# Optimization experiments

Hardware: AMD Instinct MI355X
Metric: run time of the kernel (lower is better)

The kernel has to match this reference:

```python
import jax, jax.numpy as jnp
import numpy as np

NUM_HOPS = 3
SIGMA = 0.1
EPS = 1e-12  # torch F.normalize default eps


def _l2_normalize(v):
    n = jnp.linalg.norm(v, axis=1, keepdims=True)
    return v / jnp.maximum(n, EPS)


def setup_inputs() -> dict:
    key = jax.random.key(0)
    k1, k2 = jax.random.split(key)
    N, d, E = 50000, 128, 500000
    x = jax.random.normal(k1, (N, d), dtype=jnp.float32)
    edge_index = jax.random.randint(k2, (2, E), 0, N, dtype=jnp.int64)
    return {"x": x, "edge_index": edge_index}


def reference(x, edge_index):
    N = x.shape[0]
    src, dst = edge_index[0], edge_index[1]
    noise_key = jax.random.key(42)
    h = _l2_normalize(x)
    outs = [h]
    for k in range(NUM_HOPS):
        h_src = h[src]                              # [E, d] gather
        h_dst = h[dst]                              # [E, d] gather
        alpha = jax.nn.sigmoid(jnp.sum(h_src * h_dst, axis=1))  # [E]
        # sparse.mm(alpha^T, h): out[dst] += alpha_e * h[src]
        aggr = jax.ops.segment_sum(alpha[:, None] * h_src, dst, num_segments=N)
        noise = SIGMA * jax.random.normal(jax.random.fold_in(noise_key, k), aggr.shape, aggr.dtype)
        h = _l2_normalize(aggr + noise)
        outs.append(h)
    return jnp.stack(outs)  # [num_hops+1, N, d]
```

## Files before the change

### kernel.cpp

```cpp
#include <hip/hip_runtime.h>
#include <stdint.h>

#define D 128
#define SIGMA 0.1f

typedef unsigned int uint;
typedef unsigned short ushort;

__host__ __device__ inline void tf2x32(uint32_t k0, uint32_t k1,
                                       uint32_t x0, uint32_t x1,
                                       uint32_t& o0, uint32_t& o1) {
  const uint32_t ks2 = k0 ^ k1 ^ 0x1BD11BDAu;
#define ROTL(v, r) (((v) << (r)) | ((v) >> (32 - (r))))
#define RND(R) { x0 += x1; x1 = ROTL(x1, R); x1 ^= x0; }
  x0 += k0; x1 += k1;
  RND(13) RND(15) RND(26) RND(6)
  x0 += k1; x1 += ks2 + 1u;
  RND(17) RND(29) RND(16) RND(24)
  x0 += ks2; x1 += k0 + 2u;
  RND(13) RND(15) RND(26) RND(6)
  x0 += k0; x1 += k1 + 3u;
  RND(17) RND(29) RND(16) RND(24)
  x0 += k1; x1 += ks2 + 4u;
  RND(13) RND(15) RND(26) RND(6)
  x0 += ks2; x1 += k0 + 5u;
#undef RND
#undef ROTL
  o0 = x0; o1 = x1;
}

__device__ inline float jax_normal(uint32_t k0, uint32_t k1, uint32_t idx) {
  uint32_t o0, o1;
  tf2x32(k0, k1, 0u, idx, o0, o1);
  uint32_t bits = o0 ^ o1;
  float f = __uint_as_float((bits >> 9) | 0x3f800000u) - 1.0f;
  const float lo = __uint_as_float(0xBF7FFFFFu);
  float u = fmaxf(lo, f * 2.0f + lo);
  float w = -__logf((1.0f - u) * (1.0f + u));
  float p;
  if (w < 5.0f) {
    w -= 2.5f;
    p = 2.81022636e-08f;
    p = fmaf(p, w, 3.43273939e-07f);
    p = fmaf(p, w, -3.5233877e-06f);
    p = fmaf(p, w, -4.39150654e-06f);
    p = fmaf(p, w, 0.00021858087f);
    p = fmaf(p, w, -0.00125372503f);
    p = fmaf(p, w, -0.00417768164f);
    p = fmaf(p, w, 0.246640727f);
    p = fmaf(p, w, 1.50140941f);
  } else {
    w = sqrtf(w) - 3.0f;
    p = -0.000200214257f;
    p = fmaf(p, w, 0.000100950558f);
    p = fmaf(p, w, 0.00134934322f);
    p = fmaf(p, w, -0.00367342844f);
    p = fmaf(p, w, 0.00573950773f);
    p = fmaf(p, w, -0.0076224613f);
    p = fmaf(p, w, 0.00943887047f);
    p = fmaf(p, w, 1.00167406f);
    p = fmaf(p, w, 2.83297682f);
  }
  return 1.41421356237f * (p * u);
}

__device__ inline uint bf16r(float f) {
  uint u = __float_as_uint(f);
  return (u + 0x7fffu + ((u >> 16) & 1u)) >> 16;
}

__device__ inline void unpk8(uint4 u, float* a) {
  a[0] = __uint_as_float(u.x << 16);
  a[1] = __uint_as_float(u.x & 0xffff0000u);
  a[2] = __uint_as_float(u.y << 16);
  a[3] = __uint_as_float(u.y & 0xffff0000u);
  a[4] = __uint_as_float(u.z << 16);
  a[5] = __uint_as_float(u.z & 0xffff0000u);
  a[6] = __uint_as_float(u.w << 16);
  a[7] = __uint_as_float(u.w & 0xffff0000u);
}

template<int USEB>
__device__ inline void ldrow16(const float* __restrict__ hf,
                               const uint4* __restrict__ hb,
                               int node, int sl, float* a) {
  if (USEB) {
    unpk8(hb[node * 16 + sl], a);
  } else {
    float4 v0 = ((const float4*)hf)[node * 32 + sl * 2];
    float4 v1 = ((const float4*)hf)[node * 32 + sl * 2 + 1];
    a[0] = v0.x; a[1] = v0.y; a[2] = v0.z; a[3] = v0.w;
    a[4] = v1.x; a[5] = v1.y; a[6] = v1.z; a[7] = v1.w;
  }
}

__global__ __launch_bounds__(256) void k_hist(const int* __restrict__ dst,
                                              int* __restrict__ cnt, int E) {
  int i = (blockIdx.x * blockDim.x + threadIdx.x) * 4;
  if (i + 3 < E) {
    int4 d = *(const int4*)(dst + i);
    atomicAdd(&cnt[d.x], 1);
    atomicAdd(&cnt[d.y], 1);
    atomicAdd(&cnt[d.z], 1);
    atomicAdd(&cnt[d.w], 1);
  } else {
    for (int j = i; j < E; ++j) atomicAdd(&cnt[dst[j]], 1);
  }
}

__global__ __launch_bounds__(256) void k_bsum(const int* __restrict__ cnt,
                                              int* __restrict__ bsum, int N) {
  __shared__ int ws[4];
  int b = blockIdx.x, t = threadIdx.x;
  int base = b * 1024 + t * 4;
  int4 c = {0, 0, 0, 0};
  if (base + 3 < N) c = *(const int4*)(cnt + base);
  else {
    if (base < N) c.x = cnt[base];
    if (base + 1 < N) c.y = cnt[base + 1];
    if (base + 2 < N) c.z = cnt[base + 2];
    if (base + 3 < N) c.w = cnt[base + 3];
  }
  int s = c.x + c.y + c.z + c.w;
  #pragma unroll
  for (int off = 32; off; off >>= 1) s += __shfl_xor(s, off);
  if ((t & 63) == 0) ws[t >> 6] = s;
  __syncthreads();
  if (t == 0) bsum[b] = ws[0] + ws[1] + ws[2] + ws[3];
}

__global__ void k_bscan(const int* __restrict__ bsum, int* __restrict__ boff,
                        int* __restrict__ rowN, int NB) {
  int lane = threadIdx.x;
  int carry = 0;
  for (int base = 0; base < NB; base += 64) {
    int idx = base + lane;
    int v = (idx < NB) ? bsum[idx] : 0;
    int incl = v;
    #pragma unroll
    for (int off = 1; off < 64; off <<= 1) {
      int t = __shfl_up(incl, off);
      if (lane >= off) incl += t;
    }
    if (idx < NB) boff[idx] = carry + incl - v;
    carry += __shfl(incl, 63);
  }
  if (lane == 0) rowN[0] = carry;
}

__global__ __launch_bounds__(256) void k_apply(const int* __restrict__ cnt,
                                               const int* __restrict__ boff,
                                               int* __restrict__ row,
                                               int* __restrict__ cur, int N) {
  __shared__ int wsum[4];
  int b = blockIdx.x, t = threadIdx.x;
  int base = b * 1024 + t * 4;
  int4 c = {0, 0, 0, 0};
  if (base + 3 < N) c = *(const int4*)(cnt + base);
  else {
    if (base < N) c.x = cnt[base];
    if (base + 1 < N) c.y = cnt[base + 1];
    if (base + 2 < N) c.z = cnt[base + 2];
    if (base + 3 < N) c.w = cnt[base + 3];
  }
  int s = c.x + c.y + c.z + c.w;
  int incl = s;
  #pragma unroll
  for (int off = 1; off < 64; off <<= 1) {
    int tv = __shfl_up(incl, off);
    if ((t & 63) >= off) incl += tv;
  }
  int wid = t >> 6;
  if ((t & 63) == 63) wsum[wid] = incl;
  __syncthreads();
  int woff = 0;
  for (int w = 0; w < wid; ++w) woff += wsum[w];
  int ex = boff[b] + woff + incl - s;
  int r0 = ex, r1 = ex + c.x, r2 = r1 + c.y, r3 = r2 + c.z;
  if (base + 3 < N) {
    *(int4*)(row + base) = make_int4(r0, r1, r2, r3);
    *(int4*)(cur + base) = make_int4(r0, r1, r2, r3);
  } else {
    if (base < N)     { row[base] = r0;     cur[base] = r0; }
    if (base + 1 < N) { row[base + 1] = r1; cur[base + 1] = r1; }
    if (base + 2 < N) { row[base + 2] = r2; cur[base + 2] = r2; }
  }
}

__global__ __launch_bounds__(256) void k_fill(const int* __restrict__ src,
                                              const int* __restrict__ dst,
                                              int* __restrict__ cur,
                                              int* __restrict__ csr, int E) {
  int i = (blockIdx.x * blockDim.x + threadIdx.x) * 4;
  if (i + 3 < E) {
    int4 d = *(const int4*)(dst + i);
    int4 s = *(const int4*)(src + i);
    csr[atomicAdd(&cur[d.x], 1)] = s.x;
    csr[atomicAdd(&cur[d.y], 1)] = s.y;
    csr[atomicAdd(&cur[d.z], 1)] = s.z;
    csr[atomicAdd(&cur[d.w], 1)] = s.w;
  } else {
    for (int j = i; j < E; ++j) csr[atomicAdd(&cur[dst[j]], 1)] = src[j];
  }
}

template<int USEB>
__global__ __launch_bounds__(256) void k_norm0(const float* __restrict__ x,
                                               float* __restrict__ h,
                                               uint2* __restrict__ hb, int N) {
  int gid = blockIdx.x * blockDim.x + threadIdx.x;
  int node = gid >> 5, lane = gid & 31;
  if (node >= N) return;
  float4 v = ((const float4*)x)[node * 32 + lane];
  float ss = v.x * v.x + v.y * v.y + v.z * v.z + v.w * v.w;
  #pragma unroll
  for (int off = 16; off; off >>= 1) ss += __shfl_xor(ss, off);
  float inv = 1.0f / fmaxf(sqrtf(ss), 1e-12f);
  float4 o; o.x = v.x * inv; o.y = v.y * inv; o.z = v.z * inv; o.w = v.w * inv;
  ((float4*)h)[node * 32 + lane] = o;
  if (USEB) {
    uint2 u;
    u.x = bf16r(o.x) | (bf16r(o.y) << 16);
    u.y = bf16r(o.z) | (bf16r(o.w) << 16);
    hb[node * 32 + lane] = u;
  }
}

template<int USEB>
__global__ __launch_bounds__(256) void k_hop(
    const float* __restrict__ hpf, const uint4* __restrict__ hpb,
    float* __restrict__ hof, uint* __restrict__ hob, int wb,
    const int* __restrict__ row, const int* __restrict__ csr,
    int N, uint32_t k0, uint32_t k1) {
  int gid = blockIdx.x * blockDim.x + threadIdx.x;
  int node = gid >> 6;
  if (node >= N) return;
  int lane = threadIdx.x & 63;
  int sl = lane & 15, g = lane >> 4;

  float hv[8];
  ldrow16<USEB>(hpf, hpb, node, sl, hv);
  float acc[8] = {0.f, 0.f, 0.f, 0.f, 0.f, 0.f, 0.f, 0.f};

  int b = row[node], e = row[node + 1];
  for (int cb = b; cb < e; cb += 64) {
    int cn = min(64, e - cb);
    int eidx = csr[min(cb + lane, e - 1)];
    for (int jb = 0; jb < cn; jb += 16) {
      int pos = jb + (g << 2);
      int i0 = __shfl(eidx, pos);
      int i1 = __shfl(eidx, pos + 1);
      int i2 = __shfl(eidx, pos + 2);
      int i3 = __shfl(eidx, pos + 3);
      float a0[8], a1[8], a2[8], a3[8];
      ldrow16<USEB>(hpf, hpb, i0, sl, a0);
      ldrow16<USEB>(hpf, hpb, i1, sl, a1);
      ldrow16<USEB>(hpf, hpb, i2, sl, a2);
      ldrow16<USEB>(hpf, hpb, i3, sl, a3);
      float p0 = 0.f, p1 = 0.f, p2 = 0.f, p3 = 0.f;
      #pragma unroll
      for (int t = 0; t < 8; ++t) {
        p0 = fmaf(a0[t], hv[t], p0);
        p1 = fmaf(a1[t], hv[t], p1);
        p2 = fmaf(a2[t], hv[t], p2);
        p3 = fmaf(a3[t], hv[t], p3);
      }
      #pragma unroll
      for (int off = 1; off < 16; off <<= 1) {
        p0 += __shfl_xor(p0, off);
        p1 += __shfl_xor(p1, off);
        p2 += __shfl_xor(p2, off);
        p3 += __shfl_xor(p3, off);
      }
      float al0 = (pos     < cn) ? __builtin_amdgcn_rcpf(1.0f + __expf(-p0)) : 0.f;
      float al1 = (pos + 1 < cn) ? __builtin_amdgcn_rcpf(1.0f + __expf(-p1)) : 0.f;
      float al2 = (pos + 2 < cn) ? __builtin_amdgcn_rcpf(1.0f + __expf(-p2)) : 0.f;
      float al3 = (pos + 3 < cn) ? __builtin_amdgcn_rcpf(1.0f + __expf(-p3)) : 0.f;
      #pragma unroll
      for (int t = 0; t < 8; ++t) {
        acc[t] = fmaf(al0, a0[t], acc[t]);
        acc[t] = fmaf(al1, a1[t], acc[t]);
        acc[t] = fmaf(al2, a2[t], acc[t]);
        acc[t] = fmaf(al3, a3[t], acc[t]);
      }
    }
  }

  #pragma unroll
  for (int t = 0; t < 8; ++t) {
    acc[t] += __shfl_xor(acc[t], 16);
    acc[t] += __shfl_xor(acc[t], 32);
  }

  float p0s = (g & 1) ? acc[2] : acc[0];
  float p1s = (g & 1) ? acc[3] : acc[1];
  float q0s = (g & 1) ? acc[6] : acc[4];
  float q1s = (g & 1) ? acc[7] : acc[5];
  float s0 = (g & 2) ? q0s : p0s;
  float s1 = (g & 2) ? q1s : p1s;

  uint32_t j0 = (uint32_t)node * 128u + (uint32_t)sl * 8u + (uint32_t)g * 2u;
  s0 += SIGMA * jax_normal(k0, k1, j0);
  s1 += SIGMA * jax_normal(k0, k1, j0 + 1u);

  float ss = s0 * s0 + s1 * s1;
  #pragma unroll
  for (int off = 32; off; off >>= 1) ss += __shfl_xor(ss, off);
  float inv = __builtin_amdgcn_rcpf(fmaxf(sqrtf(ss), 1e-12f));
  float o0 = s0 * inv, o1 = s1 * inv;
  int oi = node * 64 + sl * 4 + g;
  ((float2*)hof)[oi] = make_float2(o0, o1);
  if (USEB && wb) hob[oi] = bf16r(o0) | (bf16r(o1) << 16);
}

extern "C" void kernel_launch(void* const* d_in, const int* in_sizes, int n_in,
                              void* d_out, int out_size, void* d_ws, size_t ws_size,
                              hipStream_t stream) {
  const float* x = (const float*)d_in[0];
  const int* ei = (const int*)d_in[1];
  int N = in_sizes[0] / D;
  int E = in_sizes[1] / 2;
  const int* src = ei;
  const int* dst = ei + E;
  float* out = (float*)d_out;
  size_t nd = (size_t)N * D;

  int Np = (N + 3) & ~3;
  int Ep = (E + 3) & ~3;
  int NB = (N + 1023) / 1024;
  int NBp = (NB + 3) & ~3;
  int* cnt  = (int*)d_ws;
  int* row  = cnt + Np;
  int* cur  = row + Np + 4;
  int* csr  = cur + Np;
  int* bsum = csr + Ep;
  int* boff = bsum + NBp;

  size_t int_bytes = ((size_t)(3 * Np + 4 + Ep + 2 * NBp)) * 4;
  size_t hb_off = (int_bytes + 255) & ~(size_t)255;
  size_t hb_bytes = (size_t)N * D * 2;
  bool useb = ws_size >= hb_off + 2 * hb_bytes;
  ushort* hb0 = (ushort*)((char*)d_ws + hb_off);
  ushort* hb1 = hb0 + (size_t)N * D;

  hipMemsetAsync(cnt, 0, sizeof(int) * (size_t)Np, stream);
  int eb4 = (E / 4 + 256) / 256;
  k_hist<<<eb4, 256, 0, stream>>>(dst, cnt, E);
  k_bsum<<<NB, 256, 0, stream>>>(cnt, bsum, N);
  k_bscan<<<1, 64, 0, stream>>>(bsum, boff, row + N, NB);
  k_apply<<<NB, 256, 0, stream>>>(cnt, boff, row, cur, N);
  k_fill<<<eb4, 256, 0, stream>>>(src, dst, cur, csr, E);

  int nb32 = (N * 32 + 255) / 256;
  int nb64 = (N * 64 + 255) / 256;

  if (useb) {
    k_norm0<1><<<nb32, 256, 0, stream>>>(x, out, (uint2*)hb0, N);
    for (int k = 0; k < 3; ++k) {
      uint32_t ka, kb;
      tf2x32(0u, 42u, 0u, (uint32_t)k, ka, kb);
      const uint4* hin = (const uint4*)((k & 1) ? hb1 : hb0);
      uint* hout = (uint*)((k & 1) ? hb0 : hb1);
      k_hop<1><<<nb64, 256, 0, stream>>>(nullptr, hin,
                                         out + (size_t)(k + 1) * nd, hout,
                                         (k < 2) ? 1 : 0,
                                         row, csr, N, ka, kb);
    }
  } else {
    k_norm0<0><<<nb32, 256, 0, stream>>>(x, out, nullptr, N);
    for (int k = 0; k < 3; ++k) {
      uint32_t ka, kb;
      tf2x32(0u, 42u, 0u, (uint32_t)k, ka, kb);
      k_hop<0><<<nb64, 256, 0, stream>>>(out + (size_t)k * nd, nullptr,
                                         out + (size_t)(k + 1) * nd, nullptr, 0,
                                         row, csr, N, ka, kb);
    }
  }
}
```

Measured before the change: 199.3 us.

## Compute edge attention dots with bf16 MFMA and fuse CSR scan kernels

The per-edge dot products in the hop kernel now run on the 16x16x32 bf16 MFMA instruction. Each chunk loads 16 neighbour rows as the A operand and the node's row as B, replacing per-lane FMAs and shuffle reductions. The neighbour rows are also loaded a second time in a per-lane layout for the weighted accumulation, which doubles gather traffic per chunk. Separately, the block scan and apply kernels are fused into one kernel when there are at most 64 blocks, and the memset is replaced by a zeroing kernel, cutting launch count in the CSR build.

```diff
diff --git a/kernel.cpp b/kernel.cpp
--- a/kernel.cpp
+++ b/kernel.cpp
@@ -6,6 +6,11 @@
 
 typedef unsigned int uint;
 typedef unsigned short ushort;
+
+typedef short s8v __attribute__((ext_vector_type(8)));
+typedef float f32x4 __attribute__((ext_vector_type(4)));
+
+union U4S8 { uint4 u; s8v s; };
 
 __host__ __device__ inline void tf2x32(uint32_t k0, uint32_t k1,
                                        uint32_t x0, uint32_t x1,
@@ -94,6 +99,11 @@
   }
 }
 
+__global__ __launch_bounds__(256) void k_zero(int4* __restrict__ p, int n4) {
+  int i = blockIdx.x * blockDim.x + threadIdx.x;
+  if (i < n4) p[i] = make_int4(0, 0, 0, 0);
+}
+
 __global__ __launch_bounds__(256) void k_hist(const int* __restrict__ dst,
                                               int* __restrict__ cnt, int E) {
   int i = (blockIdx.x * blockDim.x + threadIdx.x) * 4;
@@ -127,6 +137,60 @@
   if ((t & 63) == 0) ws[t >> 6] = s;
   __syncthreads();
   if (t == 0) bsum[b] = ws[0] + ws[1] + ws[2] + ws[3];
+}
+
+__global__ __launch_bounds__(256) void k_apply2(const int* __restrict__ cnt,
+                                                const int* __restrict__ bsum,
+                                                int* __restrict__ row,
+                                                int* __restrict__ cur,
+                                                int N, int NB) {
+  __shared__ int sboff;
+  __shared__ int wsum[4];
+  int b = blockIdx.x, t = threadIdx.x;
+  if (t < 64) {
+    int v = (t < NB) ? bsum[t] : 0;
+    int incl = v;
+    #pragma unroll
+    for (int off = 1; off < 64; off <<= 1) {
+      int tv = __shfl_up(incl, off);
+      if (t >= off) incl += tv;
+    }
+    if (t == b) sboff = incl - v;
+    if (b == 0 && t == NB - 1) row[N] = incl;
+  }
+  __syncthreads();
+
+  int base = b * 1024 + t * 4;
+  int4 c = {0, 0, 0, 0};
+  if (base + 3 < N) c = *(const int4*)(cnt + base);
+  else {
+    if (base < N) c.x = cnt[base];
+    if (base + 1 < N) c.y = cnt[base + 1];
+    if (base + 2 < N) c.z = cnt[base + 2];
+    if (base + 3 < N) c.w = cnt[base + 3];
+  }
+  int s = c.x + c.y + c.z + c.w;
+  int incl = s;
+  #pragma unroll
+  for (int off = 1; off < 64; off <<= 1) {
+    int tv = __shfl_up(incl, off);
+    if ((t & 63) >= off) incl += tv;
+  }
+  int wid = t >> 6;
+  if ((t & 63) == 63) wsum[wid] = incl;
+  __syncthreads();
+  int woff = 0;
+  for (int w = 0; w < wid; ++w) woff += wsum[w];
+  int ex = sboff + woff + incl - s;
+  int r0 = ex, r1 = ex + c.x, r2 = r1 + c.y, r3 = r2 + c.z;
+  if (base + 3 < N) {
+    *(int4*)(row + base) = make_int4(r0, r1, r2, r3);
+    *(int4*)(cur + base) = make_int4(r0, r1, r2, r3);
+  } else {
+    if (base < N)     { row[base] = r0;     cur[base] = r0; }
+    if (base + 1 < N) { row[base + 1] = r1; cur[base + 1] = r1; }
+    if (base + 2 < N) { row[base + 2] = r2; cur[base + 2] = r2; }
+  }
 }
 
 __global__ void k_bscan(const int* __restrict__ bsum, int* __restrict__ boff,
@@ -226,9 +290,8 @@
   }
 }
 
-template<int USEB>
-__global__ __launch_bounds__(256) void k_hop(
-    const float* __restrict__ hpf, const uint4* __restrict__ hpb,
+__global__ __launch_bounds__(256) void k_hop_mfma(
+    const uint4* __restrict__ hpb,
     float* __restrict__ hof, uint* __restrict__ hob, int wb,
     const int* __restrict__ row, const int* __restrict__ csr,
     int N, uint32_t k0, uint32_t k1) {
@@ -238,10 +301,95 @@
   int lane = threadIdx.x & 63;
   int sl = lane & 15, g = lane >> 4;
 
+  int b = row[node], e = row[node + 1];
+
+  U4S8 bf0, bf1, bf2, bf3;
+  bf0.u = hpb[node * 16 + 0 * 4 + g];
+  bf1.u = hpb[node * 16 + 1 * 4 + g];
+  bf2.u = hpb[node * 16 + 2 * 4 + g];
+  bf3.u = hpb[node * 16 + 3 * 4 + g];
+
+  float acc[8] = {0.f, 0.f, 0.f, 0.f, 0.f, 0.f, 0.f, 0.f};
+
+  for (int cb = b; cb < e; cb += 16) {
+    int sA = csr[min(cb + sl, e - 1)];
+    U4S8 af0, af1, af2, af3;
+    af0.u = hpb[sA * 16 + 0 * 4 + g];
+    af1.u = hpb[sA * 16 + 1 * 4 + g];
+    af2.u = hpb[sA * 16 + 2 * 4 + g];
+    af3.u = hpb[sA * 16 + 3 * 4 + g];
+
+    int i0 = __shfl(sA, g * 4 + 0);
+    int i1 = __shfl(sA, g * 4 + 1);
+    int i2 = __shfl(sA, g * 4 + 2);
+    int i3 = __shfl(sA, g * 4 + 3);
+    uint4 u0 = hpb[i0 * 16 + sl];
+    uint4 u1 = hpb[i1 * 16 + sl];
+    uint4 u2 = hpb[i2 * 16 + sl];
+    uint4 u3 = hpb[i3 * 16 + sl];
+
+    f32x4 dfr = {0.f, 0.f, 0.f, 0.f};
+    dfr = __builtin_amdgcn_mfma_f32_16x16x32_bf16(af0.s, bf0.s, dfr, 0, 0, 0);
+    dfr = __builtin_amdgcn_mfma_f32_16x16x32_bf16(af1.s, bf1.s, dfr, 0, 0, 0);
+    dfr = __builtin_amdgcn_mfma_f32_16x16x32_bf16(af2.s, bf2.s, dfr, 0, 0, 0);
+    dfr = __builtin_amdgcn_mfma_f32_16x16x32_bf16(af3.s, bf3.s, dfr, 0, 0, 0);
+
+    float al0 = (cb + g * 4 + 0 < e) ? __builtin_amdgcn_rcpf(1.0f + __expf(-dfr[0])) : 0.f;
+    float al1 = (cb + g * 4 + 1 < e) ? __builtin_amdgcn_rcpf(1.0f + __expf(-dfr[1])) : 0.f;
+    float al2 = (cb + g * 4 + 2 < e) ? __builtin_amdgcn_rcpf(1.0f + __expf(-dfr[2])) : 0.f;
+    float al3 = (cb + g * 4 + 3 < e) ? __builtin_amdgcn_rcpf(1.0f + __expf(-dfr[3])) : 0.f;
+
+    float a0[8], a1[8], a2[8], a3[8];
+    unpk8(u0, a0); unpk8(u1, a1); unpk8(u2, a2); unpk8(u3, a3);
+    #pragma unroll
+    for (int t = 0; t < 8; ++t) {
+      acc[t] = fmaf(al0, a0[t], acc[t]);
+      acc[t] = fmaf(al1, a1[t], acc[t]);
+      acc[t] = fmaf(al2, a2[t], acc[t]);
+      acc[t] = fmaf(al3, a3[t], acc[t]);
+    }
+  }
+
+  #pragma unroll
+  for (int t = 0; t < 8; ++t) {
+    acc[t] += __shfl_xor(acc[t], 16);
+    acc[t] += __shfl_xor(acc[t], 32);
+  }
+
+  float p0s = (g & 1) ? acc[2] : acc[0];
+  float p1s = (g & 1) ? acc[3] : acc[1];
+  float q0s = (g & 1) ? acc[6] : acc[4];
+  float q1s = (g & 1) ? acc[7] : acc[5];
+  float s0 = (g & 2) ? q0s : p0s;
+  float s1 = (g & 2) ? q1s : p1s;
+
+  uint32_t j0 = (uint32_t)node * 128u + (uint32_t)sl * 8u + (uint32_t)g * 2u;
+  s0 += SIGMA * jax_normal(k0, k1, j0);
+  s1 += SIGMA * jax_normal(k0, k1, j0 + 1u);
+
+  float ss = s0 * s0 + s1 * s1;
+  #pragma unroll
+  for (int off = 32; off; off >>= 1) ss += __shfl_xor(ss, off);
+  float inv = __builtin_amdgcn_rcpf(fmaxf(sqrtf(ss), 1e-12f));
+  float o0 = s0 * inv, o1 = s1 * inv;
+  int oi = node * 64 + sl * 4 + g;
+  ((float2*)hof)[oi] = make_float2(o0, o1);
+  if (wb) hob[oi] = bf16r(o0) | (bf16r(o1) << 16);
+}
+
+__global__ __launch_bounds__(256) void k_hop_f32(
+    const float* __restrict__ hpf, float* __restrict__ hof,
+    const int* __restrict__ row, const int* __restrict__ csr,
+    int N, uint32_t k0, uint32_t k1) {
+  int gid = blockIdx.x * blockDim.x + threadIdx.x;
+  int node = gid >> 6;
+  if (node >= N) return;
+  int lane = threadIdx.x & 63;
+  int sl = lane & 15, g = lane >> 4;
+
   float hv[8];
-  ldrow16<USEB>(hpf, hpb, node, sl, hv);
+  ldrow16<0>(hpf, nullptr, node, sl, hv);
   float acc[8] = {0.f, 0.f, 0.f, 0.f, 0.f, 0.f, 0.f, 0.f};
-
   int b = row[node], e = row[node + 1];
   for (int cb = b; cb < e; cb += 64) {
     int cn = min(64, e - cb);
@@ -253,10 +401,10 @@
       int i2 = __shfl(eidx, pos + 2);
       int i3 = __shfl(eidx, pos + 3);
       float a0[8], a1[8], a2[8], a3[8];
-      ldrow16<USEB>(hpf, hpb, i0, sl, a0);
-      ldrow16<USEB>(hpf, hpb, i1, sl, a1);
-      ldrow16<USEB>(hpf, hpb, i2, sl, a2);
-      ldrow16<USEB>(hpf, hpb, i3, sl, a3);
+      ldrow16<0>(hpf, nullptr, i0, sl, a0);
+      ldrow16<0>(hpf, nullptr, i1, sl, a1);
+      ldrow16<0>(hpf, nullptr, i2, sl, a2);
+      ldrow16<0>(hpf, nullptr, i3, sl, a3);
       float p0 = 0.f, p1 = 0.f, p2 = 0.f, p3 = 0.f;
       #pragma unroll
       for (int t = 0; t < 8; ++t) {
@@ -285,13 +433,11 @@
       }
     }
   }
-
   #pragma unroll
   for (int t = 0; t < 8; ++t) {
     acc[t] += __shfl_xor(acc[t], 16);
     acc[t] += __shfl_xor(acc[t], 32);
   }
-
   float p0s = (g & 1) ? acc[2] : acc[0];
   float p1s = (g & 1) ? acc[3] : acc[1];
   float q0s = (g & 1) ? acc[6] : acc[4];
@@ -310,7 +456,6 @@
   float o0 = s0 * inv, o1 = s1 * inv;
   int oi = node * 64 + sl * 4 + g;
   ((float2*)hof)[oi] = make_float2(o0, o1);
-  if (USEB && wb) hob[oi] = bf16r(o0) | (bf16r(o1) << 16);
 }
 
 extern "C" void kernel_launch(void* const* d_in, const int* in_sizes, int n_in,
@@ -343,12 +488,17 @@
   ushort* hb0 = (ushort*)((char*)d_ws + hb_off);
   ushort* hb1 = hb0 + (size_t)N * D;
 
-  hipMemsetAsync(cnt, 0, sizeof(int) * (size_t)Np, stream);
+  int n4 = Np / 4;
+  k_zero<<<(n4 + 255) / 256, 256, 0, stream>>>((int4*)cnt, n4);
   int eb4 = (E / 4 + 256) / 256;
   k_hist<<<eb4, 256, 0, stream>>>(dst, cnt, E);
   k_bsum<<<NB, 256, 0, stream>>>(cnt, bsum, N);
-  k_bscan<<<1, 64, 0, stream>>>(bsum, boff, row + N, NB);
-  k_apply<<<NB, 256, 0, stream>>>(cnt, boff, row, cur, N);
+  if (NB <= 64) {
+    k_apply2<<<NB, 256, 0, stream>>>(cnt, bsum, row, cur, N, NB);
+  } else {
+    k_bscan<<<1, 64, 0, stream>>>(bsum, boff, row + N, NB);
+    k_apply<<<NB, 256, 0, stream>>>(cnt, boff, row, cur, N);
+  }
   k_fill<<<eb4, 256, 0, stream>>>(src, dst, cur, csr, E);
 
   int nb32 = (N * 32 + 255) / 256;
@@ -361,19 +511,19 @@
       tf2x32(0u, 42u, 0u, (uint32_t)k, ka, kb);
       const uint4* hin = (const uint4*)((k & 1) ? hb1 : hb0);
       uint* hout = (uint*)((k & 1) ? hb0 : hb1);
-      k_hop<1><<<nb64, 256, 0, stream>>>(nullptr, hin,
-                                         out + (size_t)(k + 1) * nd, hout,
-                                         (k < 2) ? 1 : 0,
-                                         row, csr, N, ka, kb);
+      k_hop_mfma<<<nb64, 256, 0, stream>>>(hin,
+                                           out + (size_t)(k + 1) * nd, hout,
+                                           (k < 2) ? 1 : 0,
+                                           row, csr, N, ka, kb);
     }
   } else {
     k_norm0<0><<<nb32, 256, 0, stream>>>(x, out, nullptr, N);
     for (int k = 0; k < 3; ++k) {
       uint32_t ka, kb;
       tf2x32(0u, 42u, 0u, (uint32_t)k, ka, kb);
-      k_hop<0><<<nb64, 256, 0, stream>>>(out + (size_t)k * nd, nullptr,
-                                         out + (size_t)(k + 1) * nd, nullptr, 0,
-                                         row, csr, N, ka, kb);
+      k_hop_f32<<<nb64, 256, 0, stream>>>(out + (size_t)k * nd,
+                                          out + (size_t)(k + 1) * nd,
+                                          row, csr, N, ka, kb);
     }
   }
 }
```

New measurement: 207.0 us. 1.04x slower.
